# Kernel optimization log

Measured on AMD Instinct MI355X. Metric: run time of the kernel, lower is better.

Reference implementation:

```python
import jax, jax.numpy as jnp
import numpy as np

T, B, IN_DIM, MEM_DIM = 256, 64, 512, 512


def _kaiming(key, shape):
    # kaiming_normal_ default: fan_in = shape[1], gain = sqrt(2)
    std = np.sqrt(2.0 / shape[1])
    return jax.random.normal(key, shape, dtype=jnp.float32) * std


def setup_inputs() -> dict:
    key = jax.random.key(0)
    ks = jax.random.split(key, 10)
    inp = {
        "inputs": jax.random.normal(ks[0], (T, B, IN_DIM), dtype=jnp.float32),
        "emb_s": jax.random.normal(ks[1], (T, B, IN_DIM), dtype=jnp.float32),
        "c0": jnp.zeros((B, MEM_DIM), dtype=jnp.float32),
        "h0": jnp.zeros((B, MEM_DIM), dtype=jnp.float32),
        # learned params (torch Linear: y = x @ W.T + b)
        "W_ioux": _kaiming(ks[2], (4 * MEM_DIM, IN_DIM)),
        "b_ioux": jnp.zeros((4 * MEM_DIM,), jnp.float32),
        "W_iouh": _kaiming(ks[3], (4 * MEM_DIM, MEM_DIM)),
        "b_iouh": jnp.zeros((4 * MEM_DIM,), jnp.float32),
        "W_ious": _kaiming(ks[4], (4 * MEM_DIM, IN_DIM)),
        "b_ious": jnp.zeros((4 * MEM_DIM,), jnp.float32),
        "W_fx": _kaiming(ks[5], (MEM_DIM, IN_DIM)),
        "b_fx": jnp.zeros((MEM_DIM,), jnp.float32),
        "W_fh": _kaiming(ks[6], (MEM_DIM, MEM_DIM)),
        "b_fh": jnp.zeros((MEM_DIM,), jnp.float32),
        "W_wc": _kaiming(ks[7], (MEM_DIM, IN_DIM)),
        "b_wc": jnp.zeros((MEM_DIM,), jnp.float32),
    }
    return inp


def reference(inputs, emb_s, c0, h0,
              W_ioux, b_ioux, W_iouh, b_iouh, W_ious, b_ious,
              W_fx, b_fx, W_fh, b_fh, W_wc, b_wc):
    M = W_fh.shape[0]
    # Precompute all input-dependent projections for the whole sequence (big GEMMs).
    iou_x = (jnp.einsum('tbi,gi->tbg', inputs, W_ioux) + b_ioux
             + jnp.einsum('tbi,gi->tbg', emb_s, W_ious) + b_ious)      # [T,B,4M]
    ctelta_x = jnp.einsum('tbi,mi->tbm', inputs, W_fx) + b_fx          # [T,B,M]
    wc_s = jnp.tanh(jnp.einsum('tbi,mi->tbm', emb_s, W_wc) + b_wc)    # [T,B,M]

    def step(carry, xs):
        c, h = carry
        iou_t, ctx_t, wcs_t = xs
        iou = iou_t + h @ W_iouh.T + b_iouh                            # [B,4M]
        f, i, o, o_c = jnp.split(jax.nn.sigmoid(iou), 4, axis=1)
        c_telta = jnp.tanh(ctx_t + h @ W_fh.T + b_fh)
        c_new = i * c_telta + f * c
        h_new = o * jnp.tanh(c_new) + o_c * wcs_t
        return (c_new, h_new), h_new

    (c_fin, h_fin), out = jax.lax.scan(step, (c0, h0), (iou_x, ctelta_x, wc_s))
    return out, (c_fin, h_fin)
```

## Files before the change

kernel.cpp:

```cpp
#include <hip/hip_runtime.h>
#include <stdint.h>

#define T_STEPS 256
#define B_DIM   64
#define MDIM    512
#define NROWS   (T_STEPS * B_DIM)
#define KCAT    1024
#define NBIG    3072
#define W2ROWS  2560
#define NBLK2   32
#define OUT_N   ((size_t)T_STEPS * B_DIM * MDIM)

typedef short v8s __attribute__((ext_vector_type(8)));
typedef float v4f __attribute__((ext_vector_type(4)));

static __device__ __forceinline__ unsigned short f2bf(float f) {
    unsigned u = __builtin_bit_cast(unsigned, f);
    u += 0x7FFFu + ((u >> 16) & 1u);
    return (unsigned short)(u >> 16);
}
static __device__ __forceinline__ float bf2f(unsigned short h) {
    unsigned u = ((unsigned)h) << 16;
    return __builtin_bit_cast(float, u);
}
static __device__ __forceinline__ float sigmoidf(float x) {
    return 1.0f / (1.0f + __expf(-x));
}


__global__ void pack_xcat(const float* __restrict__ x, const float* __restrict__ s,
                          unsigned short* __restrict__ xcat) {
    int idx = blockIdx.x * blockDim.x + threadIdx.x;
    if (idx >= NROWS * KCAT) return;
    int row = idx >> 10, col = idx & 1023;
    float v = (col < 512) ? x[row * 512 + col] : s[row * 512 + (col - 512)];
    xcat[idx] = f2bf(v);
}

__global__ void pack_wbig(const float* __restrict__ Wioux, const float* __restrict__ bioux,
                          const float* __restrict__ Wious, const float* __restrict__ bious,
                          const float* __restrict__ Wfx,   const float* __restrict__ bfx,
                          const float* __restrict__ Wwc,   const float* __restrict__ bwc,
                          unsigned short* __restrict__ wbig, float* __restrict__ bbig) {
    int idx = blockIdx.x * blockDim.x + threadIdx.x;
    if (idx >= NBIG * KCAT) return;
    int r = idx >> 10, c = idx & 1023;
    float v;
    if (r < 2048)      v = (c < 512) ? Wioux[r * 512 + c] : Wious[r * 512 + (c - 512)];
    else if (r < 2560) { int j = r - 2048; v = (c < 512) ? Wfx[j * 512 + c] : 0.0f; }
    else               { int j = r - 2560; v = (c < 512) ? 0.0f : Wwc[j * 512 + (c - 512)]; }
    wbig[idx] = f2bf(v);
    if (c == 0) {
        float b;
        if (r < 2048)      b = bioux[r] + bious[r];
        else if (r < 2560) b = bfx[r - 2048];
        else               b = bwc[r - 2560];
        bbig[r] = b;
    }
}

__global__ void pack_w2(const float* __restrict__ Wiouh, const float* __restrict__ biouh,
                        const float* __restrict__ Wfh,   const float* __restrict__ bfh,
                        unsigned short* __restrict__ w2, float* __restrict__ b2) {
    int idx = blockIdx.x * blockDim.x + threadIdx.x;
    if (idx >= W2ROWS * 512) return;
    int r = idx >> 9, k = idx & 511;
    int bk = r / 80, rem = r % 80, g = rem >> 4, j = rem & 15;
    int m = bk * 16 + j;
    float v, bias;
    if (g < 4) { v = Wiouh[(size_t)(g * 512 + m) * 512 + k]; bias = biouh[g * 512 + m]; }
    else       { v = Wfh[(size_t)m * 512 + k];               bias = bfh[m]; }
    w2[idx] = f2bf(v);
    if (k == 0) b2[r] = bias;
}

__global__ void init_state(const float* __restrict__ h0,
                           unsigned short* __restrict__ hbuf0,
                           int* __restrict__ cnt) {
    int idx = blockIdx.x * blockDim.x + threadIdx.x;
    if (idx >= B_DIM * MDIM) return;
    hbuf0[idx] = f2bf(h0[idx]);
    if (idx == 0) *cnt = 0;
}


__global__ __launch_bounds__(256) void gemm_big(
        const unsigned short* __restrict__ xcat,
        const unsigned short* __restrict__ wbig,
        const float* __restrict__ bbig,
        unsigned short* __restrict__ yall) {
    __shared__ __align__(16) unsigned short As[128][40];
    __shared__ __align__(16) unsigned short Bs[128][40];
    int nb = blockIdx.x;
    int mb = blockIdx.y;
    int tid = threadIdx.x;
    int lane = tid & 63, wid = tid >> 6;
    int wm = wid & 1, wn = wid >> 1;
    int lm = lane & 15, lq = lane >> 4;
    v4f acc[4][4] = {};
    for (int kb = 0; kb < KCAT / 32; ++kb) {
        __syncthreads();
        #pragma unroll
        for (int it = 0; it < 2; ++it) {
            int cid = tid + it * 256;
            int r = cid >> 2, q = cid & 3;
            *(uint4*)&As[r][q * 8] =
                *(const uint4*)(xcat + (size_t)(mb * 128 + r) * KCAT + kb * 32 + q * 8);
            *(uint4*)&Bs[r][q * 8] =
                *(const uint4*)(wbig + (size_t)(nb * 128 + r) * KCAT + kb * 32 + q * 8);
        }
        __syncthreads();
        v8s a[4], b[4];
        #pragma unroll
        for (int i = 0; i < 4; ++i) a[i] = *(const v8s*)&As[wm * 64 + i * 16 + lm][lq * 8];
        #pragma unroll
        for (int j = 0; j < 4; ++j) b[j] = *(const v8s*)&Bs[wn * 64 + j * 16 + lm][lq * 8];
        #pragma unroll
        for (int i = 0; i < 4; ++i)
            #pragma unroll
            for (int j = 0; j < 4; ++j)
                acc[i][j] = __builtin_amdgcn_mfma_f32_16x16x32_bf16(a[i], b[j], acc[i][j], 0, 0, 0);
    }
    #pragma unroll
    for (int i = 0; i < 4; ++i) {
        int gm = mb * 128 + wm * 64 + i * 16 + lq * 4;
        #pragma unroll
        for (int j = 0; j < 4; ++j) {
            int gn = nb * 128 + wn * 64 + j * 16 + lm;
            float bias = bbig[gn];
            bool do_tanh = (gn >= 2560);
            #pragma unroll
            for (int r = 0; r < 4; ++r) {
                float v = acc[i][j][r] + bias;
                if (do_tanh) v = tanhf(v);
                yall[(size_t)(gm + r) * NBIG + gn] = f2bf(v);
            }
        }
    }
}


__device__ __forceinline__ void grid_barrier(int* cnt, int target) {
    __syncthreads();
    if (threadIdx.x == 0) {
        __hip_atomic_fetch_add(cnt, 1, __ATOMIC_ACQ_REL, __HIP_MEMORY_SCOPE_AGENT);
        while (__hip_atomic_load(cnt, __ATOMIC_ACQUIRE, __HIP_MEMORY_SCOPE_AGENT) < target)
            __builtin_amdgcn_s_sleep(1);
    }
    __syncthreads();
}

__global__ __launch_bounds__(256, 1) void lstm_persist(
        const unsigned short* __restrict__ yall,
        const unsigned short* __restrict__ w2,
        const float* __restrict__ b2,
        const float* __restrict__ c0,
        unsigned short* __restrict__ hbuf0,
        unsigned short* __restrict__ hbuf1,
        float* __restrict__ out,
        int* __restrict__ cnt) {
    __shared__ __align__(16) float red[2][10][256];
    __shared__ __align__(16) unsigned short ybuf[2][64][6][16];
    int bk = blockIdx.x;
    int tid = threadIdx.x;
    int lane = tid & 63, wid = tid >> 6;
    int p = wid >> 1;
    int q = wid & 1;
    int lm = lane & 15, lq = lane >> 4;
    int m = bk * 16 + lm;

    v8s bfrag[5][8];
    const unsigned short* w2b = w2 + (size_t)(bk * 80 + lm) * 512 + lq * 8;
    #pragma unroll
    for (int g = 0; g < 5; ++g)
        #pragma unroll
        for (int j = 0; j < 8; ++j)
            bfrag[g][j] = *(const v8s*)(w2b + (size_t)g * 16 * 512 + (q * 8 + j) * 32);

    float bias[5];
    #pragma unroll
    for (int g = 0; g < 5; ++g) bias[g] = b2[(bk * 5 + g) * 16 + lm];
    float creg[2][4];
    #pragma unroll
    for (int tb = 0; tb < 2; ++tb)
        #pragma unroll
        for (int r = 0; r < 4; ++r)
            creg[tb][r] = c0[(p * 32 + tb * 16 + lq * 4 + r) * 512 + m];

    if (q == 1) {
        #pragma unroll
        for (int i = 0; i < 6; ++i) {
            int c = (p * 6 + i) * 64 + lane;
            int b = c / 12, rem = c % 12, g = rem >> 1, half = rem & 1;
            int gcol = (g < 4) ? g * 512 : (g == 4 ? 2048 : 2560);
            const unsigned short* gp = yall + (size_t)b * NBIG + gcol + bk * 16 + half * 8;
            unsigned short* lp = &ybuf[0][0][0][0] + (p * 6 + i) * 512;
            __builtin_amdgcn_global_load_lds(
                (const __attribute__((address_space(1))) unsigned int*)gp,
                (__attribute__((address_space(3))) unsigned int*)lp, 16, 0, 0);
        }
    }

    for (int t = 0; t < T_STEPS; ++t) {
        const unsigned short* hin = (t & 1) ? hbuf1 : hbuf0;
        unsigned short*      hout = (t & 1) ? hbuf0 : hbuf1;
        v4f acc[2][5] = {};
        const unsigned short* ha = hin + (size_t)(p * 32 + lm) * 512 + q * 256 + lq * 8;
        #pragma unroll
        for (int j = 0; j < 8; ++j) {
            v8s a0 = *(const v8s*)(ha + j * 32);
            v8s a1 = *(const v8s*)(ha + 16 * 512 + j * 32);
            #pragma unroll
            for (int g = 0; g < 5; ++g) {
                acc[0][g] = __builtin_amdgcn_mfma_f32_16x16x32_bf16(a0, bfrag[g][j], acc[0][g], 0, 0, 0);
                acc[1][g] = __builtin_amdgcn_mfma_f32_16x16x32_bf16(a1, bfrag[g][j], acc[1][g], 0, 0, 0);
            }
        }
        if (q == 1) {
            #pragma unroll
            for (int tb = 0; tb < 2; ++tb)
                #pragma unroll
                for (int g = 0; g < 5; ++g)
                    *(v4f*)&red[p][tb * 5 + g][lane * 4] = acc[tb][g];
        }
        __syncthreads();
        if (q == 0) {
            #pragma unroll
            for (int tb = 0; tb < 2; ++tb)
                #pragma unroll
                for (int g = 0; g < 5; ++g)
                    acc[tb][g] += *(const v4f*)&red[p][tb * 5 + g][lane * 4];
            const unsigned short* yb = &ybuf[t & 1][0][0][0];
            #pragma unroll
            for (int tb = 0; tb < 2; ++tb) {
                #pragma unroll
                for (int r = 0; r < 4; ++r) {
                    int brow = p * 32 + tb * 16 + lq * 4 + r;
                    const unsigned short* ybr = yb + brow * 96;
                    float f_ = sigmoidf(bf2f(ybr[0 * 16 + lm]) + acc[tb][0][r] + bias[0]);
                    float i_ = sigmoidf(bf2f(ybr[1 * 16 + lm]) + acc[tb][1][r] + bias[1]);
                    float o_ = sigmoidf(bf2f(ybr[2 * 16 + lm]) + acc[tb][2][r] + bias[2]);
                    float oc = sigmoidf(bf2f(ybr[3 * 16 + lm]) + acc[tb][3][r] + bias[3]);
                    float ct = tanhf  (bf2f(ybr[4 * 16 + lm]) + acc[tb][4][r] + bias[4]);
                    float wcs = bf2f(ybr[5 * 16 + lm]);
                    float cn = i_ * ct + f_ * creg[tb][r];
                    creg[tb][r] = cn;
                    float hn = o_ * tanhf(cn) + oc * wcs;
                    out[((size_t)t * 64 + brow) * 512 + m] = hn;
                    hout[brow * 512 + m] = f2bf(hn);
                    if (t == T_STEPS - 1)
                        out[OUT_N + 32768 + (size_t)brow * 512 + m] = hn;
                }
            }
        } else if (t + 1 < T_STEPS) {
            int buf = (t + 1) & 1;
            #pragma unroll
            for (int i = 0; i < 6; ++i) {
                int c = (p * 6 + i) * 64 + lane;
                int b = c / 12, rem = c % 12, g = rem >> 1, half = rem & 1;
                int gcol = (g < 4) ? g * 512 : (g == 4 ? 2048 : 2560);
                const unsigned short* gp = yall + ((size_t)(t + 1) * 64 + b) * NBIG + gcol + bk * 16 + half * 8;
                unsigned short* lp = &ybuf[buf][0][0][0] + (p * 6 + i) * 512;
                __builtin_amdgcn_global_load_lds(
                    (const __attribute__((address_space(1))) unsigned int*)gp,
                    (__attribute__((address_space(3))) unsigned int*)lp, 16, 0, 0);
            }
        }
        grid_barrier(cnt, NBLK2 * (t + 1));
    }

    if (q == 0) {
        #pragma unroll
        for (int tb = 0; tb < 2; ++tb)
            #pragma unroll
            for (int r = 0; r < 4; ++r)
                out[OUT_N + (size_t)(p * 32 + tb * 16 + lq * 4 + r) * 512 + m] = creg[tb][r];
    }
}


extern "C" void kernel_launch(void* const* d_in, const int* in_sizes, int n_in,
                              void* d_out, int out_size, void* d_ws, size_t ws_size,
                              hipStream_t stream) {
    const float* inputs = (const float*)d_in[0];
    const float* emb_s  = (const float*)d_in[1];
    const float* c0     = (const float*)d_in[2];
    const float* h0     = (const float*)d_in[3];
    const float* W_ioux = (const float*)d_in[4];  const float* b_ioux = (const float*)d_in[5];
    const float* W_iouh = (const float*)d_in[6];  const float* b_iouh = (const float*)d_in[7];
    const float* W_ious = (const float*)d_in[8];  const float* b_ious = (const float*)d_in[9];
    const float* W_fx   = (const float*)d_in[10]; const float* b_fx   = (const float*)d_in[11];
    const float* W_fh   = (const float*)d_in[12]; const float* b_fh   = (const float*)d_in[13];
    const float* W_wc   = (const float*)d_in[14]; const float* b_wc   = (const float*)d_in[15];
    float* out = (float*)d_out;

    char* ws = (char*)d_ws;
    size_t off = 0;
    auto alloc = [&](size_t bytes) -> void* {
        void* p = ws + off;
        off += (bytes + 255) & ~(size_t)255;
        return p;
    };
    unsigned short* yall  = (unsigned short*)alloc((size_t)NROWS * NBIG * 2);
    unsigned short* xcat  = (unsigned short*)alloc((size_t)NROWS * KCAT * 2);
    unsigned short* wbig  = (unsigned short*)alloc((size_t)NBIG * KCAT * 2);
    float*          bbig  = (float*)alloc(NBIG * 4);
    unsigned short* w2    = (unsigned short*)alloc((size_t)W2ROWS * 512 * 2);
    float*          b2    = (float*)alloc(W2ROWS * 4);
    unsigned short* hbuf0 = (unsigned short*)alloc(B_DIM * MDIM * 2);
    unsigned short* hbuf1 = (unsigned short*)alloc(B_DIM * MDIM * 2);
    int*            cnt   = (int*)alloc(256);

    pack_xcat<<<(NROWS * KCAT + 255) / 256, 256, 0, stream>>>(inputs, emb_s, xcat);
    pack_wbig<<<(NBIG * KCAT + 255) / 256, 256, 0, stream>>>(
        W_ioux, b_ioux, W_ious, b_ious, W_fx, b_fx, W_wc, b_wc, wbig, bbig);
    pack_w2<<<(W2ROWS * 512 + 255) / 256, 256, 0, stream>>>(W_iouh, b_iouh, W_fh, b_fh, w2, b2);
    init_state<<<(B_DIM * MDIM + 255) / 256, 256, 0, stream>>>(h0, hbuf0, cnt);

    dim3 g1(NBIG / 128, NROWS / 128);
    gemm_big<<<g1, 256, 0, stream>>>(xcat, wbig, bbig, yall);

    lstm_persist<<<NBLK2, 256, 0, stream>>>(yall, w2, b2, c0, hbuf0, hbuf1, out, cnt);
}
```

Before: 2.318 ms.

## Replace grid barrier with per-block flags and tile h and projection layouts

Swaps the atomic-counter grid barrier for per-block step flags: each wave polls all 32 flags with a wave-wide vote before reading h. h is now kept in a slab layout (16-column chunks per block), staged through LDS and written with 64-bit relaxed atomic stores. The big GEMM writes its output pre-tiled per timestep and block, so each block's per-step projection slice is one contiguous 12KB chunk, and that prefetch is issued at the start of the step. The aim is to cut barrier latency and scattered loads on the serial recurrence. The price is relaxed memory ordering with only a vmcnt wait and no explicit release fence, which risks stale reads. Reuse of the double buffer is also only ordered through the flags.

```diff
diff --git a/kernel.cpp b/kernel.cpp
--- a/kernel.cpp
+++ b/kernel.cpp
@@ -13,6 +13,7 @@
 
 typedef short v8s __attribute__((ext_vector_type(8)));
 typedef float v4f __attribute__((ext_vector_type(4)));
+typedef unsigned long long u64;
 
 static __device__ __forceinline__ unsigned short f2bf(float f) {
     unsigned u = __builtin_bit_cast(unsigned, f);
@@ -75,12 +76,13 @@
 }
 
 __global__ void init_state(const float* __restrict__ h0,
-                           unsigned short* __restrict__ hbuf0,
-                           int* __restrict__ cnt) {
+                           unsigned short* __restrict__ hslab0,
+                           int* __restrict__ flags) {
     int idx = blockIdx.x * blockDim.x + threadIdx.x;
+    if (idx < NBLK2) flags[idx] = 0;
     if (idx >= B_DIM * MDIM) return;
-    hbuf0[idx] = f2bf(h0[idx]);
-    if (idx == 0) *cnt = 0;
+    int row = idx >> 9, col = idx & 511;
+    hslab0[((col >> 4) * 64 + row) * 16 + (col & 15)] = f2bf(h0[idx]);
 }
 
 
@@ -88,7 +90,7 @@
         const unsigned short* __restrict__ xcat,
         const unsigned short* __restrict__ wbig,
         const float* __restrict__ bbig,
-        unsigned short* __restrict__ yall) {
+        unsigned short* __restrict__ ytile) {
     __shared__ __align__(16) unsigned short As[128][40];
     __shared__ __align__(16) unsigned short Bs[128][40];
     int nb = blockIdx.x;
@@ -121,46 +123,44 @@
             for (int j = 0; j < 4; ++j)
                 acc[i][j] = __builtin_amdgcn_mfma_f32_16x16x32_bf16(a[i], b[j], acc[i][j], 0, 0, 0);
     }
+    int tt = mb * 2 + wm;
     #pragma unroll
     for (int i = 0; i < 4; ++i) {
-        int gm = mb * 128 + wm * 64 + i * 16 + lq * 4;
+        int rbase = i * 16 + lq * 4;
         #pragma unroll
         for (int j = 0; j < 4; ++j) {
             int gn = nb * 128 + wn * 64 + j * 16 + lm;
             float bias = bbig[gn];
             bool do_tanh = (gn >= 2560);
+            int slot, mcol;
+            if (gn < 2048)      { slot = gn >> 9; mcol = gn & 511; }
+            else if (gn < 2560) { slot = 4; mcol = gn - 2048; }
+            else                { slot = 5; mcol = gn - 2560; }
+            size_t base = ((((size_t)tt * NBLK2 + (mcol >> 4)) * 64 + rbase) * 6 + slot) * 16
+                          + (mcol & 15);
             #pragma unroll
             for (int r = 0; r < 4; ++r) {
                 float v = acc[i][j][r] + bias;
                 if (do_tanh) v = tanhf(v);
-                yall[(size_t)(gm + r) * NBIG + gn] = f2bf(v);
-            }
-        }
-    }
-}
-
-
-__device__ __forceinline__ void grid_barrier(int* cnt, int target) {
-    __syncthreads();
-    if (threadIdx.x == 0) {
-        __hip_atomic_fetch_add(cnt, 1, __ATOMIC_ACQ_REL, __HIP_MEMORY_SCOPE_AGENT);
-        while (__hip_atomic_load(cnt, __ATOMIC_ACQUIRE, __HIP_MEMORY_SCOPE_AGENT) < target)
-            __builtin_amdgcn_s_sleep(1);
-    }
-    __syncthreads();
-}
+                ytile[base + (size_t)r * 96] = f2bf(v);
+            }
+        }
+    }
+}
+
 
 __global__ __launch_bounds__(256, 1) void lstm_persist(
-        const unsigned short* __restrict__ yall,
+        const unsigned short* __restrict__ ytile,
         const unsigned short* __restrict__ w2,
         const float* __restrict__ b2,
         const float* __restrict__ c0,
-        unsigned short* __restrict__ hbuf0,
-        unsigned short* __restrict__ hbuf1,
+        unsigned short* hslab0,
+        unsigned short* hslab1,
         float* __restrict__ out,
-        int* __restrict__ cnt) {
+        int* __restrict__ flags) {
     __shared__ __align__(16) float red[2][10][256];
-    __shared__ __align__(16) unsigned short ybuf[2][64][6][16];
+    __shared__ __align__(16) unsigned short ybuf[2][6144];
+    __shared__ __align__(16) unsigned short hstage[64][16];
     int bk = blockIdx.x;
     int tid = threadIdx.x;
     int lane = tid & 63, wid = tid >> 6;
@@ -188,32 +188,59 @@
             creg[tb][r] = c0[(p * 32 + tb * 16 + lq * 4 + r) * 512 + m];
 
     if (q == 1) {
+        const unsigned short* slab = ytile + (size_t)bk * 6144;
         #pragma unroll
         for (int i = 0; i < 6; ++i) {
-            int c = (p * 6 + i) * 64 + lane;
-            int b = c / 12, rem = c % 12, g = rem >> 1, half = rem & 1;
-            int gcol = (g < 4) ? g * 512 : (g == 4 ? 2048 : 2560);
-            const unsigned short* gp = yall + (size_t)b * NBIG + gcol + bk * 16 + half * 8;
-            unsigned short* lp = &ybuf[0][0][0][0] + (p * 6 + i) * 512;
+            int ch = p * 6 + i;
             __builtin_amdgcn_global_load_lds(
-                (const __attribute__((address_space(1))) unsigned int*)gp,
-                (__attribute__((address_space(3))) unsigned int*)lp, 16, 0, 0);
+                (const __attribute__((address_space(1))) unsigned int*)(slab + ch * 512 + lane * 8),
+                (__attribute__((address_space(3))) unsigned int*)(&ybuf[0][0] + ch * 512), 16, 0, 0);
         }
     }
 
     for (int t = 0; t < T_STEPS; ++t) {
-        const unsigned short* hin = (t & 1) ? hbuf1 : hbuf0;
-        unsigned short*      hout = (t & 1) ? hbuf0 : hbuf1;
+        int cur = t & 1;
+        if (q == 1 && t + 1 < T_STEPS) {
+            const unsigned short* slab = ytile + (size_t)((t + 1) * NBLK2 + bk) * 6144;
+            unsigned short* lbase = &ybuf[cur ^ 1][0];
+            #pragma unroll
+            for (int i = 0; i < 6; ++i) {
+                int ch = p * 6 + i;
+                __builtin_amdgcn_global_load_lds(
+                    (const __attribute__((address_space(1))) unsigned int*)(slab + ch * 512 + lane * 8),
+                    (__attribute__((address_space(3))) unsigned int*)(lbase + ch * 512), 16, 0, 0);
+            }
+        }
+        if (t) {
+            int slot = lane & 31;
+            while (!__all(__hip_atomic_load(flags + slot, __ATOMIC_RELAXED,
+                                            __HIP_MEMORY_SCOPE_AGENT) >= t)) {}
+            asm volatile("" ::: "memory");
+        }
+        const u64* hin = cur ? (const u64*)hslab1 : (const u64*)hslab0;
+        u64*       hnx = cur ? (u64*)hslab0 : (u64*)hslab1;
+        u64 hq[32];
+        {
+            const u64* hb = hin + ((size_t)(q * 16 + (lq >> 1)) * 64 + p * 32 + lm) * 4
+                          + (lq & 1) * 2;
+            #pragma unroll
+            for (int j = 0; j < 8; ++j) {
+                hq[j * 4 + 0] = __hip_atomic_load(hb + j * 512,      __ATOMIC_RELAXED, __HIP_MEMORY_SCOPE_AGENT);
+                hq[j * 4 + 1] = __hip_atomic_load(hb + j * 512 + 1,  __ATOMIC_RELAXED, __HIP_MEMORY_SCOPE_AGENT);
+                hq[j * 4 + 2] = __hip_atomic_load(hb + j * 512 + 64, __ATOMIC_RELAXED, __HIP_MEMORY_SCOPE_AGENT);
+                hq[j * 4 + 3] = __hip_atomic_load(hb + j * 512 + 65, __ATOMIC_RELAXED, __HIP_MEMORY_SCOPE_AGENT);
+            }
+        }
         v4f acc[2][5] = {};
-        const unsigned short* ha = hin + (size_t)(p * 32 + lm) * 512 + q * 256 + lq * 8;
         #pragma unroll
         for (int j = 0; j < 8; ++j) {
-            v8s a0 = *(const v8s*)(ha + j * 32);
-            v8s a1 = *(const v8s*)(ha + 16 * 512 + j * 32);
+            union { u64 qq[2]; v8s v; } a0, a1;
+            a0.qq[0] = hq[j * 4 + 0]; a0.qq[1] = hq[j * 4 + 1];
+            a1.qq[0] = hq[j * 4 + 2]; a1.qq[1] = hq[j * 4 + 3];
             #pragma unroll
             for (int g = 0; g < 5; ++g) {
-                acc[0][g] = __builtin_amdgcn_mfma_f32_16x16x32_bf16(a0, bfrag[g][j], acc[0][g], 0, 0, 0);
-                acc[1][g] = __builtin_amdgcn_mfma_f32_16x16x32_bf16(a1, bfrag[g][j], acc[1][g], 0, 0, 0);
+                acc[0][g] = __builtin_amdgcn_mfma_f32_16x16x32_bf16(a0.v, bfrag[g][j], acc[0][g], 0, 0, 0);
+                acc[1][g] = __builtin_amdgcn_mfma_f32_16x16x32_bf16(a1.v, bfrag[g][j], acc[1][g], 0, 0, 0);
             }
         }
         if (q == 1) {
@@ -230,7 +257,7 @@
                 #pragma unroll
                 for (int g = 0; g < 5; ++g)
                     acc[tb][g] += *(const v4f*)&red[p][tb * 5 + g][lane * 4];
-            const unsigned short* yb = &ybuf[t & 1][0][0][0];
+            const unsigned short* yb = &ybuf[cur][0];
             #pragma unroll
             for (int tb = 0; tb < 2; ++tb) {
                 #pragma unroll
@@ -247,26 +274,26 @@
                     creg[tb][r] = cn;
                     float hn = o_ * tanhf(cn) + oc * wcs;
                     out[((size_t)t * 64 + brow) * 512 + m] = hn;
-                    hout[brow * 512 + m] = f2bf(hn);
+                    hstage[brow][lm] = f2bf(hn);
                     if (t == T_STEPS - 1)
                         out[OUT_N + 32768 + (size_t)brow * 512 + m] = hn;
                 }
             }
-        } else if (t + 1 < T_STEPS) {
-            int buf = (t + 1) & 1;
-            #pragma unroll
-            for (int i = 0; i < 6; ++i) {
-                int c = (p * 6 + i) * 64 + lane;
-                int b = c / 12, rem = c % 12, g = rem >> 1, half = rem & 1;
-                int gcol = (g < 4) ? g * 512 : (g == 4 ? 2048 : 2560);
-                const unsigned short* gp = yall + ((size_t)(t + 1) * 64 + b) * NBIG + gcol + bk * 16 + half * 8;
-                unsigned short* lp = &ybuf[buf][0][0][0] + (p * 6 + i) * 512;
-                __builtin_amdgcn_global_load_lds(
-                    (const __attribute__((address_space(1))) unsigned int*)gp,
-                    (__attribute__((address_space(3))) unsigned int*)lp, 16, 0, 0);
-            }
-        }
-        grid_barrier(cnt, NBLK2 * (t + 1));
+        }
+        __syncthreads();
+        if (wid == 0) {
+            const u64* hsl = (const u64*)&hstage[0][0];
+            u64* dst = hnx + (size_t)bk * 256;
+            u64 x0 = hsl[lane * 4 + 0], x1 = hsl[lane * 4 + 1];
+            u64 x2 = hsl[lane * 4 + 2], x3 = hsl[lane * 4 + 3];
+            __hip_atomic_store(dst + lane * 4 + 0, x0, __ATOMIC_RELAXED, __HIP_MEMORY_SCOPE_AGENT);
+            __hip_atomic_store(dst + lane * 4 + 1, x1, __ATOMIC_RELAXED, __HIP_MEMORY_SCOPE_AGENT);
+            __hip_atomic_store(dst + lane * 4 + 2, x2, __ATOMIC_RELAXED, __HIP_MEMORY_SCOPE_AGENT);
+            __hip_atomic_store(dst + lane * 4 + 3, x3, __ATOMIC_RELAXED, __HIP_MEMORY_SCOPE_AGENT);
+            asm volatile("s_waitcnt vmcnt(0)" ::: "memory");
+            if (lane == 0 && t + 1 < T_STEPS)
+                __hip_atomic_store(flags + bk, t + 1, __ATOMIC_RELAXED, __HIP_MEMORY_SCOPE_AGENT);
+        }
     }
 
     if (q == 0) {
@@ -301,24 +328,24 @@
         off += (bytes + 255) & ~(size_t)255;
         return p;
     };
-    unsigned short* yall  = (unsigned short*)alloc((size_t)NROWS * NBIG * 2);
+    unsigned short* ytile = (unsigned short*)alloc((size_t)NROWS * NBIG * 2);
     unsigned short* xcat  = (unsigned short*)alloc((size_t)NROWS * KCAT * 2);
     unsigned short* wbig  = (unsigned short*)alloc((size_t)NBIG * KCAT * 2);
     float*          bbig  = (float*)alloc(NBIG * 4);
     unsigned short* w2    = (unsigned short*)alloc((size_t)W2ROWS * 512 * 2);
     float*          b2    = (float*)alloc(W2ROWS * 4);
-    unsigned short* hbuf0 = (unsigned short*)alloc(B_DIM * MDIM * 2);
-    unsigned short* hbuf1 = (unsigned short*)alloc(B_DIM * MDIM * 2);
-    int*            cnt   = (int*)alloc(256);
+    unsigned short* hslab0 = (unsigned short*)alloc(B_DIM * MDIM * 2);
+    unsigned short* hslab1 = (unsigned short*)alloc(B_DIM * MDIM * 2);
+    int*            flags  = (int*)alloc(256);
 
     pack_xcat<<<(NROWS * KCAT + 255) / 256, 256, 0, stream>>>(inputs, emb_s, xcat);
     pack_wbig<<<(NBIG * KCAT + 255) / 256, 256, 0, stream>>>(
         W_ioux, b_ioux, W_ious, b_ious, W_fx, b_fx, W_wc, b_wc, wbig, bbig);
     pack_w2<<<(W2ROWS * 512 + 255) / 256, 256, 0, stream>>>(W_iouh, b_iouh, W_fh, b_fh, w2, b2);
-    init_state<<<(B_DIM * MDIM + 255) / 256, 256, 0, stream>>>(h0, hbuf0, cnt);
+    init_state<<<(B_DIM * MDIM + 255) / 256, 256, 0, stream>>>(h0, hslab0, flags);
 
     dim3 g1(NBIG / 128, NROWS / 128);
-    gemm_big<<<g1, 256, 0, stream>>>(xcat, wbig, bbig, yall);
-
-    lstm_persist<<<NBLK2, 256, 0, stream>>>(yall, w2, b2, c0, hbuf0, hbuf1, out, cnt);
-}
+    gemm_big<<<g1, 256, 0, stream>>>(xcat, wbig, bbig, ytile);
+
+    lstm_persist<<<NBLK2, 256, 0, stream>>>(ytile, w2, b2, c0, hslab0, hslab1, out, flags);
+}
```

New measurement: 2.628 ms. 13.4% more time.
